# Optimization experiments

Hardware: AMD Instinct MI355X
Metric: run time of the kernel (lower is better)

## Reference

```python
import jax, jax.numpy as jnp
import numpy as np

MAX_VAL = 255.0
C1 = (0.01 * MAX_VAL) ** 2
C2 = (0.03 * MAX_VAL) ** 2


def _gauss_window(ws, sigma, channel=3):
    x = np.arange(ws, dtype=np.float64)
    g = np.exp(-((x - ws // 2) ** 2) / (2.0 * sigma ** 2))
    g = g / g.sum()
    w2 = np.outer(g, g).astype(np.float32)  # [ws, ws]
    w = np.broadcast_to(w2, (channel, 1, ws, ws)).copy()  # depthwise OIHW
    return jnp.asarray(w)


def _dwconv(x, w, pad):
    # depthwise conv2d, NCHW, groups == channels
    return jax.lax.conv_general_dilated(
        x, w, window_strides=(1, 1), padding=[(pad, pad), (pad, pad)],
        dimension_numbers=("NCHW", "OIHW", "NCHW"),
        feature_group_count=x.shape[1])


def _ssim_pair(img1, img2):
    _, c, h, w = img1.shape
    ws = min(h, w, 11)
    sigma = 1.5 * ws / 11.0
    win = _gauss_window(ws, sigma, c)
    pad = ws // 2
    mu1 = _dwconv(img1, win, pad)
    mu2 = _dwconv(img2, win, pad)
    mu1_sq, mu2_sq, mu1_mu2 = mu1 * mu1, mu2 * mu2, mu1 * mu2
    sigma1_sq = _dwconv(img1 * img1, win, pad) - mu1_sq
    sigma2_sq = _dwconv(img2 * img2, win, pad) - mu2_sq
    sigma12 = _dwconv(img1 * img2, win, pad) - mu1_mu2
    V1 = 2.0 * sigma12 + C2
    V2 = sigma1_sq + sigma2_sq + C2
    ssim_map = (2.0 * mu1_mu2 + C1) * V1 / ((mu1_sq + mu2_sq + C1) * V2)
    mcs_map = V1 / V2
    return ssim_map.mean(), mcs_map.mean()


def _avg_pool2(x):
    B, C, H, W = x.shape
    return x.reshape(B, C, H // 2, 2, W // 2, 2).mean(axis=(3, 5))


def _ms_ssim(img1, img2, levels=5):
    weight = jnp.array([0.0448, 0.2856, 0.3001, 0.2363, 0.1333], jnp.float32)
    msssim, mcs = [], []
    for _ in range(levels):
        s, m = _ssim_pair(img1, img2)
        msssim.append(s)
        mcs.append(m)
        img1 = _avg_pool2(img1)
        img2 = _avg_pool2(img2)
    msssim = jnp.stack(msssim)
    mcs = jnp.stack(mcs)
    value = jnp.prod(mcs[: levels - 1] ** weight[: levels - 1]) * msssim[levels - 1] ** weight[levels - 1]
    return 1.0 - value


def _l1_oss(img1, img2):
    _, c, h, w = img1.shape
    ws = min(h, w, 7)
    sigma = 1.1 * ws / 7.0
    win = _gauss_window(ws, sigma, c)
    return _dwconv(jnp.abs(img1 - img2), win, ws // 2).mean()


def _clr_loss(img1, img3):
    _, c, h, w = img1.shape
    ws = min(h, w, 29)
    sigma = ws / 6.0
    win = _gauss_window(ws, sigma, c)
    pad = ws // 2
    mu1 = _dwconv(img1, win, pad)
    mu3 = _dwconv(img3, win, pad)
    cw = [-0.000519, 0.07633, -0.173433, 1.435936, -1.894404, 1.556091]
    # Horner evaluation of cw[5]*x^5 + ... + cw[1]*x + cw[0]
    mu1 = ((((cw[5] * mu1 + cw[4]) * mu1 + cw[3]) * mu1 + cw[2]) * mu1 + cw[1]) * mu1 + cw[0]
    wgray = jnp.array([0.299, 0.587, 0.144], jnp.float32).reshape(1, 3, 1, 1)
    mug1 = (mu1 * wgray).sum(axis=1, keepdims=True)  # 1x1 conv over channels
    mug3 = (mu3 * wgray).sum(axis=1, keepdims=True)
    me1 = mug1.mean(axis=(2, 3), keepdims=True)
    me3 = mug3.mean(axis=(2, 3), keepdims=True)
    sc = me1 / me3
    return jnp.abs(mu1 - mu3 * sc).mean()


def setup_inputs() -> dict:
    key = jax.random.key(0)
    k1, k2, k3 = jax.random.split(key, 3)
    shape = (16, 3, 512, 512)
    return {
        "img1": jax.random.uniform(k1, shape, dtype=jnp.float32),
        "img2": jax.random.uniform(k2, shape, dtype=jnp.float32),
        "img3": jax.random.uniform(k3, shape, dtype=jnp.float32),
    }


def reference(img1, img2, img3):
    l1v = _l1_oss(img1, img2)
    clrv = _clr_loss(img1, img3)
    ssimv = _ms_ssim(img1, img2)
    return 0.4 * ssimv + 0.4 * l1v + 0.2 * clrv
```

## Files before the change

kernel.cpp:

```cpp
#include <hip/hip_runtime.h>
#include <hip/hip_fp16.h>
#include <cmath>

typedef float f2 __attribute__((ext_vector_type(2)));

struct GW7  { float g[7];  };
struct GW11 { float g[11]; };
struct GW29 { float g[29]; };

static void make_gauss(int ws, double sigma, float* out) {
    double t[32]; double s = 0.0;
    int c = ws / 2;
    for (int i = 0; i < ws; ++i) { double d = i - c; t[i] = exp(-(d * d) / (2.0 * sigma * sigma)); s += t[i]; }
    for (int i = 0; i < ws; ++i) out[i] = (float)(t[i] / s);
}

#define ACC_SLOTS 44
#define ACC_BYTES (ACC_SLOTS * 64 * sizeof(double))

__device__ __forceinline__ float poly5(float x) {
    float r = fmaf(1.556091f, x, -1.894404f);
    r = fmaf(r, x, 1.435936f);
    r = fmaf(r, x, -0.173433f);
    r = fmaf(r, x, 0.07633f);
    r = fmaf(r, x, -0.000519f);
    return r;
}

__device__ __forceinline__ float border7(int p, const GW7& gw) {
    if (p >= 3 && p <= 508) return 1.f;
    float r = 0.f;
    #pragma unroll
    for (int k = 0; k < 7; ++k) { int q = p + 3 - k; if (q >= 0 && q < 512) r += gw.g[k]; }
    return r;
}

#define SSP 49
#define SRP 33
template<bool INTER>
__global__ __launch_bounds__(256) void ssim_kernel(
    const float* __restrict__ Aim, const float* __restrict__ Bim, const f2* __restrict__ AB,
    int H, int tpp, int tilesX, GW11 gw, GW7 g7, double* __restrict__ acc, int level,
    f2* __restrict__ pooled, int Ho)
{
    constexpr int TILE = 32, IN = 42;
    __shared__ f2 lds[2 * IN * SRP];
    __shared__ float red[12];
    f2* s    = lds;
    f2* r_mu = lds;
    f2* r_sq = lds + IN * SRP;

    const int tid = threadIdx.x;
    const int bid = blockIdx.x;
    const int plane = bid / tpp;
    const int t = bid - plane * tpp;
    const int ty = t / tilesX, tx = t - ty * tilesX;
    const size_t base = (size_t)plane * H * H;
    const int oy = ty * TILE - 5, ox = tx * TILE - 5;

    for (int i = tid; i < IN * IN; i += 256) {
        int y = i / IN, x = i - y * IN;
        int gy = oy + y, gx = ox + x;
        bool ok = (gy >= 0) && (gy < H) && (gx >= 0) && (gx < H);
        size_t o = base + (size_t)gy * H + gx;
        f2 v = {0.f, 0.f};
        if (ok) {
            if (INTER) v = AB[o];
            else { v.x = Aim[o]; v.y = Bim[o]; }
        }
        s[y * SSP + x] = v;
    }
    __syncthreads();

    f2 v[18];
    const int ry = tid >> 2, rx0 = (tid & 3) * 8;
    if (tid < IN * 4) {
        #pragma unroll
        for (int l = 0; l < 18; ++l) v[l] = s[ry * SSP + rx0 + l];
    }
    if (pooled) {
        int py = tid >> 4, px = tid & 15;
        int a = (5 + 2 * py) * SSP + 5 + 2 * px;
        f2 u = s[a] + s[a + 1] + s[a + SSP] + s[a + SSP + 1];
        pooled[(size_t)plane * Ho * Ho + (size_t)(ty * 16 + py) * Ho + (tx * 16 + px)] = 0.25f * u;
    }
    float l1p = 0.f;
    if (level == 0) {
        #pragma unroll
        for (int jj = 0; jj < 4; ++jj) {
            int p = jj * 256 + tid;
            int py = p >> 5, px = p & 31;
            f2 u = s[(5 + py) * SSP + 5 + px];
            float w = border7(ty * 32 + py, g7) * border7(tx * 32 + px, g7);
            l1p += w * fabsf(u.x - u.y);
        }
    }
    __syncthreads();

    if (tid < IN * 4) {
        #pragma unroll
        for (int j = 0; j < 8; ++j) {
            f2 a = {0.f, 0.f};
            #pragma unroll
            for (int k = 0; k < 11; ++k) a = gw.g[k] * v[j + k] + a;
            r_mu[ry * SRP + rx0 + j] = a;
        }
        #pragma unroll
        for (int l = 0; l < 18; ++l) {
            f2 w;
            w.x = fmaf(v[l].x, v[l].x, v[l].y * v[l].y);
            w.y = v[l].x * v[l].y;
            v[l] = w;
        }
        #pragma unroll
        for (int j = 0; j < 8; ++j) {
            f2 a = {0.f, 0.f};
            #pragma unroll
            for (int k = 0; k < 11; ++k) a = gw.g[k] * v[j + k] + a;
            r_sq[ry * SRP + rx0 + j] = a;
        }
    }
    __syncthreads();

    const int y0 = (tid >> 5) * 4, x = tid & 31;
    float lss = 0.f, lmc = 0.f;
    {
        f2 mu[4], q[4];
        {
            f2 u[14];
            #pragma unroll
            for (int l = 0; l < 14; ++l) u[l] = r_mu[(y0 + l) * SRP + x];
            #pragma unroll
            for (int j = 0; j < 4; ++j) {
                f2 a = {0.f, 0.f};
                #pragma unroll
                for (int k = 0; k < 11; ++k) a = gw.g[k] * u[j + k] + a;
                mu[j] = a;
            }
        }
        {
            f2 u[14];
            #pragma unroll
            for (int l = 0; l < 14; ++l) u[l] = r_sq[(y0 + l) * SRP + x];
            #pragma unroll
            for (int j = 0; j < 4; ++j) {
                f2 a = {0.f, 0.f};
                #pragma unroll
                for (int k = 0; k < 11; ++k) a = gw.g[k] * u[j + k] + a;
                q[j] = a;
            }
        }
        #pragma unroll
        for (int j = 0; j < 4; ++j) {
            float m1 = mu[j].x, m2 = mu[j].y;
            float P = m1 * m2;
            float S = fmaf(m1, m1, m2 * m2);
            float V1 = 2.f * (q[j].y - P) + 58.5225f;
            float V2 = (q[j].x - S) + 58.5225f;
            float num = (2.f * P + 6.5025f) * V1;
            float SC = S + 6.5025f;
            float inv = __builtin_amdgcn_rcpf(SC * V2);
            lss = fmaf(num, inv, lss);
            lmc = fmaf(V1 * SC, inv, lmc);
        }
    }
    #pragma unroll
    for (int o = 32; o > 0; o >>= 1) {
        lss += __shfl_down(lss, o); lmc += __shfl_down(lmc, o); l1p += __shfl_down(l1p, o);
    }
    if ((tid & 63) == 0) {
        int g = tid >> 6;
        red[g * 3] = lss; red[g * 3 + 1] = lmc; red[g * 3 + 2] = l1p;
    }
    __syncthreads();
    if (tid == 0) {
        float a = red[0] + red[3] + red[6] + red[9];
        float m = red[1] + red[4] + red[7] + red[10];
        int stripe = bid & 63;
        atomicAdd(&acc[(0 + level) * 64 + stripe], (double)a);
        atomicAdd(&acc[(5 + level) * 64 + stripe], (double)m);
        if (level == 0) {
            float l1 = red[2] + red[5] + red[8] + red[11];
            atomicAdd(&acc[10 * 64 + stripe], (double)l1);
        }
    }
}

#define CRP 33
template<int MODE>
__global__ __launch_bounds__(256) void clr_conv(
    const float* __restrict__ img1, const float* __restrict__ img3,
    __half2* __restrict__ pbuf, GW29 gw, double* __restrict__ acc)
{
    __shared__ f2 r[60 * CRP];
    __shared__ float red[8];
    __shared__ float sc_sh;

    const int tid = threadIdx.x, bid = blockIdx.x;
    const int plane = bid >> 8, t = bid & 255;
    const int ty = t >> 4, tx = t & 15;
    const int b = plane / 3, c = plane - b * 3;
    const float wg = (c == 0) ? 0.299f : (c == 1 ? 0.587f : 0.144f);
    const size_t base = (size_t)plane * (512 * 512);

    if (MODE == 2 && tid < 64) {
        double m1 = acc[(12 + b) * 64 + tid];
        double m3 = acc[(28 + b) * 64 + tid];
        #pragma unroll
        for (int o = 32; o > 0; o >>= 1) { m1 += __shfl_down(m1, o); m3 += __shfl_down(m3, o); }
        if (tid == 0) sc_sh = (float)(m1 / m3);
    }

    if (tid < 240) {
        const int ry = tid >> 2, xq = tid & 3;
        const int gy = ty * 32 - 14 + ry;
        const bool vr = (gy >= 0) && (gy < 512);
        const int c0 = tx * 8 + xq * 2 - 4;
        const float4* row1 = (const float4*)(img1 + base + (size_t)(vr ? gy : 0) * 512);
        const float4* row3 = (const float4*)(img3 + base + (size_t)(vr ? gy : 0) * 512);
        float w[40];
        float o1[8];
        #pragma unroll
        for (int k = 0; k < 10; ++k) {
            int cc = c0 + k;
            float4 f = {0.f, 0.f, 0.f, 0.f};
            if (vr && cc >= 0 && cc < 128) f = row1[cc];
            w[4 * k] = f.x; w[4 * k + 1] = f.y; w[4 * k + 2] = f.z; w[4 * k + 3] = f.w;
        }
        #pragma unroll
        for (int j = 0; j < 8; ++j) {
            float a = 0.f;
            #pragma unroll
            for (int k = 0; k < 29; ++k) a = fmaf(gw.g[k], w[2 + j + k], a);
            o1[j] = a;
        }
        #pragma unroll
        for (int k = 0; k < 10; ++k) {
            int cc = c0 + k;
            float4 f = {0.f, 0.f, 0.f, 0.f};
            if (vr && cc >= 0 && cc < 128) f = row3[cc];
            w[4 * k] = f.x; w[4 * k + 1] = f.y; w[4 * k + 2] = f.z; w[4 * k + 3] = f.w;
        }
        #pragma unroll
        for (int j = 0; j < 8; ++j) {
            float a = 0.f;
            #pragma unroll
            for (int k = 0; k < 29; ++k) a = fmaf(gw.g[k], w[2 + j + k], a);
            r[ry * CRP + xq * 8 + j] = (f2){o1[j], a};
        }
    }
    __syncthreads();

    const int y0 = (tid >> 5) * 4, x = tid & 31;
    f2 mu[4];
    {
        f2 u[32];
        #pragma unroll
        for (int l = 0; l < 32; ++l) u[l] = r[(y0 + l) * CRP + x];
        #pragma unroll
        for (int j = 0; j < 4; ++j) {
            f2 a = {0.f, 0.f};
            #pragma unroll
            for (int k = 0; k < 29; ++k) a = gw.g[k] * u[j + k] + a;
            mu[j] = a;
        }
    }
    float p1 = 0.f, p3 = 0.f;
    #pragma unroll
    for (int j = 0; j < 4; ++j) {
        float p = poly5(mu[j].x);
        if (MODE == 2) {
            p1 += fabsf(p - mu[j].y * sc_sh);
        } else {
            p1 += p; p3 += mu[j].y;
            if (MODE == 0)
                pbuf[base + (size_t)(ty * 32 + y0 + j) * 512 + (tx * 32 + x)] =
                    __floats2half2_rn(p, mu[j].y);
        }
    }
    if (MODE != 2) { p1 *= wg; p3 *= wg; }
    #pragma unroll
    for (int o = 32; o > 0; o >>= 1) { p1 += __shfl_down(p1, o); p3 += __shfl_down(p3, o); }
    if ((tid & 63) == 0) { red[(tid >> 6) * 2] = p1; red[(tid >> 6) * 2 + 1] = p3; }
    __syncthreads();
    if (tid == 0) {
        float a1 = red[0] + red[2] + red[4] + red[6];
        int stripe = bid & 63;
        if (MODE == 2) {
            atomicAdd(&acc[11 * 64 + stripe], (double)a1);
        } else {
            float a3 = red[1] + red[3] + red[5] + red[7];
            atomicAdd(&acc[(12 + b) * 64 + stripe], (double)a1);
            atomicAdd(&acc[(28 + b) * 64 + stripe], (double)a3);
        }
    }
}

__global__ __launch_bounds__(256) void clr_fin(
    const __half2* __restrict__ pbuf, double* __restrict__ acc)
{
    __shared__ float red[4];
    __shared__ float sc_sh;
    const int tid = threadIdx.x, bid = blockIdx.x;
    const int b = bid / 192, sub = bid - b * 192;
    if (tid < 64) {
        double m1 = acc[(12 + b) * 64 + tid];
        double m3 = acc[(28 + b) * 64 + tid];
        #pragma unroll
        for (int o = 32; o > 0; o >>= 1) { m1 += __shfl_down(m1, o); m3 += __shfl_down(m3, o); }
        if (tid == 0) sc_sh = (float)(m1 / m3);
    }
    __syncthreads();
    const float sc = sc_sh;
    const size_t bo = (size_t)b * 786432 + (size_t)sub * 4096;
    float s = 0.f;
    #pragma unroll
    for (int it = 0; it < 8; ++it) {
        size_t i = bo + it * 512 + tid * 2;
        float2 a = __half22float2(pbuf[i]);
        float2 c = __half22float2(pbuf[i + 1]);
        s += fabsf(a.x - a.y * sc) + fabsf(c.x - c.y * sc);
    }
    #pragma unroll
    for (int o = 32; o > 0; o >>= 1) s += __shfl_down(s, o);
    if ((tid & 63) == 0) red[tid >> 6] = s;
    __syncthreads();
    if (tid == 0)
        atomicAdd(&acc[11 * 64 + (bid & 63)], (double)(red[0] + red[1] + red[2] + red[3]));
}

__global__ void finalize_kernel(const double* __restrict__ acc, float* __restrict__ out)
{
    __shared__ double sums[ACC_SLOTS];
    int t = threadIdx.x;
    if (t < ACC_SLOTS) {
        double s = 0.0;
        for (int i = 0; i < 64; ++i) s += acc[t * 64 + i];
        sums[t] = s;
    }
    __syncthreads();
    if (t == 0) {
        const double w[5] = {0.0448, 0.2856, 0.3001, 0.2363, 0.1333};
        double value = 1.0;
        for (int l = 0; l < 5; ++l) {
            double dim = (double)(512 >> l);
            double cnt = 48.0 * dim * dim;
            double mval = (l < 4) ? (sums[5 + l] / cnt) : (sums[l] / cnt);
            value *= pow(mval, w[l]);
        }
        double n0 = 48.0 * 512.0 * 512.0;
        double l1v = sums[10] / n0;
        double clrv = sums[11] / n0;
        out[0] = (float)(0.4 * (1.0 - value) + 0.4 * l1v + 0.2 * clrv);
    }
}

extern "C" void kernel_launch(void* const* d_in, const int* in_sizes, int n_in,
                              void* d_out, int out_size, void* d_ws, size_t ws_size,
                              hipStream_t stream)
{
    (void)in_sizes; (void)n_in; (void)out_size;
    const float* img1 = (const float*)d_in[0];
    const float* img2 = (const float*)d_in[1];
    const float* img3 = (const float*)d_in[2];
    float* out = (float*)d_out;
    double* acc = (double*)d_ws;

    GW11 g11; make_gauss(11, 1.5, g11.g);
    GW7  g7;  make_gauss(7, 1.1, g7.g);
    GW29 g29; make_gauss(29, 29.0 / 6.0, g29.g);

    hipMemsetAsync(d_ws, 0, ACC_BYTES, stream);

    f2* pyr = (f2*)((char*)d_ws + 32768);
    size_t offs[4];
    offs[0] = 0;
    offs[1] = offs[0] + (size_t)48 * 256 * 256;
    offs[2] = offs[1] + (size_t)48 * 128 * 128;
    offs[3] = offs[2] + (size_t)48 * 64 * 64;
    const size_t PYRF2 = offs[3] + (size_t)48 * 32 * 32;

    const f2* cur = nullptr;
    int H = 512;
    for (int l = 0; l < 5; ++l) {
        int tilesX = H / 32; int tpp = tilesX * tilesX;
        f2* pooled = (l < 4) ? (pyr + offs[l]) : nullptr;
        int Ho = H / 2;
        if (l == 0)
            ssim_kernel<false><<<48 * tpp, 256, 0, stream>>>(
                img1, img2, nullptr, H, tpp, tilesX, g11, g7, acc, l, pooled, Ho);
        else
            ssim_kernel<true><<<48 * tpp, 256, 0, stream>>>(
                nullptr, nullptr, cur, H, tpp, tilesX, g11, g7, acc, l, pooled, Ho);
        cur = pooled; H = Ho;
    }

    const size_t poff = 32768 + PYRF2 * sizeof(f2);
    const size_t PBYTES = (size_t)48 * 512 * 512 * sizeof(__half2);
    __half2* pbuf = (__half2*)((char*)d_ws + poff);
    if (ws_size >= poff + PBYTES) {
        clr_conv<0><<<12288, 256, 0, stream>>>(img1, img3, pbuf, g29, acc);
        clr_fin<<<3072, 256, 0, stream>>>(pbuf, acc);
    } else {
        clr_conv<1><<<12288, 256, 0, stream>>>(img1, img3, pbuf, g29, acc);
        clr_conv<2><<<12288, 256, 0, stream>>>(img1, img3, pbuf, g29, acc);
    }

    finalize_kernel<<<1, 64, 0, stream>>>(acc, out);
}
```

Baseline: 237.2 us.

## Stream clr conv over full column strips with a ring buffer to avoid halo recompute

Each block of the 29-tap color-loss convolution now processes a whole 32-wide column strip. It slides down 512 rows and keeps horizontally convolved rows in a 128-row shared-memory ring buffer, instead of recomputing a 28-row halo for every 32x32 tile. This removes most of the redundant horizontal convolution work and global reads. In exchange the grid shrinks from 12288 to 768 blocks, adds per-chunk barriers, and uses more shared memory, which reduces parallelism and latency hiding.

```diff
diff --git a/kernel.cpp b/kernel.cpp
--- a/kernel.cpp
+++ b/kernel.cpp
@@ -187,18 +187,18 @@
 }
 
 #define CRP 33
+#define RING 128
 template<int MODE>
 __global__ __launch_bounds__(256) void clr_conv(
     const float* __restrict__ img1, const float* __restrict__ img3,
     __half2* __restrict__ pbuf, GW29 gw, double* __restrict__ acc)
 {
-    __shared__ f2 r[60 * CRP];
+    __shared__ f2 r[RING * CRP];
     __shared__ float red[8];
     __shared__ float sc_sh;
 
     const int tid = threadIdx.x, bid = blockIdx.x;
-    const int plane = bid >> 8, t = bid & 255;
-    const int ty = t >> 4, tx = t & 15;
+    const int plane = bid >> 4, tx = bid & 15;
     const int b = plane / 3, c = plane - b * 3;
     const float wg = (c == 0) ? 0.299f : (c == 1 ? 0.587f : 0.144f);
     const size_t base = (size_t)plane * (512 * 512);
@@ -211,20 +211,25 @@
         if (tid == 0) sc_sh = (float)(m1 / m3);
     }
 
-    if (tid < 240) {
-        const int ry = tid >> 2, xq = tid & 3;
-        const int gy = ty * 32 - 14 + ry;
-        const bool vr = (gy >= 0) && (gy < 512);
-        const int c0 = tx * 8 + xq * 2 - 4;
-        const float4* row1 = (const float4*)(img1 + base + (size_t)(vr ? gy : 0) * 512);
-        const float4* row3 = (const float4*)(img3 + base + (size_t)(vr ? gy : 0) * 512);
+    const int rrow = tid >> 2, xq = tid & 3;
+    const int c0 = tx * 8 + xq * 2 - 4;
+
+    auto rowconv = [&](int lr) {
+        const int ri = ((lr + RING) & (RING - 1)) * CRP + xq * 8;
+        if (lr < 0 || lr >= 512) {
+            #pragma unroll
+            for (int j = 0; j < 8; ++j) r[ri + j] = (f2){0.f, 0.f};
+            return;
+        }
+        const float4* row1 = (const float4*)(img1 + base + (size_t)lr * 512);
+        const float4* row3 = (const float4*)(img3 + base + (size_t)lr * 512);
         float w[40];
         float o1[8];
         #pragma unroll
         for (int k = 0; k < 10; ++k) {
             int cc = c0 + k;
             float4 f = {0.f, 0.f, 0.f, 0.f};
-            if (vr && cc >= 0 && cc < 128) f = row1[cc];
+            if (cc >= 0 && cc < 128) f = row1[cc];
             w[4 * k] = f.x; w[4 * k + 1] = f.y; w[4 * k + 2] = f.z; w[4 * k + 3] = f.w;
         }
         #pragma unroll
@@ -238,7 +243,7 @@
         for (int k = 0; k < 10; ++k) {
             int cc = c0 + k;
             float4 f = {0.f, 0.f, 0.f, 0.f};
-            if (vr && cc >= 0 && cc < 128) f = row3[cc];
+            if (cc >= 0 && cc < 128) f = row3[cc];
             w[4 * k] = f.x; w[4 * k + 1] = f.y; w[4 * k + 2] = f.z; w[4 * k + 3] = f.w;
         }
         #pragma unroll
@@ -246,38 +251,48 @@
             float a = 0.f;
             #pragma unroll
             for (int k = 0; k < 29; ++k) a = fmaf(gw.g[k], w[2 + j + k], a);
-            r[ry * CRP + xq * 8 + j] = (f2){o1[j], a};
-        }
-    }
-    __syncthreads();
-
-    const int y0 = (tid >> 5) * 4, x = tid & 31;
-    f2 mu[4];
-    {
-        f2 u[32];
-        #pragma unroll
-        for (int l = 0; l < 32; ++l) u[l] = r[(y0 + l) * CRP + x];
-        #pragma unroll
-        for (int j = 0; j < 4; ++j) {
-            f2 a = {0.f, 0.f};
-            #pragma unroll
-            for (int k = 0; k < 29; ++k) a = gw.g[k] * u[j + k] + a;
-            mu[j] = a;
-        }
-    }
+            r[ri + j] = (f2){o1[j], a};
+        }
+    };
+
+    rowconv(-14 + rrow);
+    __syncthreads();
+
     float p1 = 0.f, p3 = 0.f;
-    #pragma unroll
-    for (int j = 0; j < 4; ++j) {
-        float p = poly5(mu[j].x);
-        if (MODE == 2) {
-            p1 += fabsf(p - mu[j].y * sc_sh);
-        } else {
-            p1 += p; p3 += mu[j].y;
-            if (MODE == 0)
-                pbuf[base + (size_t)(ty * 32 + y0 + j) * 512 + (tx * 32 + x)] =
-                    __floats2half2_rn(p, mu[j].y);
-        }
-    }
+    const int x = tid & 31;
+    #pragma unroll 1
+    for (int ck = 0; ck < 8; ++ck) {
+        {
+            int lr = 50 + 64 * ck + rrow;
+            if (lr <= 525) rowconv(lr);
+        }
+        __syncthreads();
+        #pragma unroll
+        for (int g = 0; g < 2; ++g) {
+            const int y0 = 64 * ck + g * 32 + (tid >> 5) * 4;
+            f2 u[32];
+            #pragma unroll
+            for (int l = 0; l < 32; ++l)
+                u[l] = r[(((y0 - 14 + l) + RING) & (RING - 1)) * CRP + x];
+            #pragma unroll
+            for (int j = 0; j < 4; ++j) {
+                f2 a = {0.f, 0.f};
+                #pragma unroll
+                for (int k = 0; k < 29; ++k) a = gw.g[k] * u[j + k] + a;
+                float p = poly5(a.x);
+                if (MODE == 2) {
+                    p1 += fabsf(p - a.y * sc_sh);
+                } else {
+                    p1 += p; p3 += a.y;
+                    if (MODE == 0)
+                        pbuf[base + (size_t)(y0 + j) * 512 + (tx * 32 + x)] =
+                            __floats2half2_rn(p, a.y);
+                }
+            }
+        }
+        if (ck < 7) __syncthreads();
+    }
+
     if (MODE != 2) { p1 *= wg; p3 *= wg; }
     #pragma unroll
     for (int o = 32; o > 0; o >>= 1) { p1 += __shfl_down(p1, o); p3 += __shfl_down(p3, o); }
@@ -399,11 +414,11 @@
     const size_t PBYTES = (size_t)48 * 512 * 512 * sizeof(__half2);
     __half2* pbuf = (__half2*)((char*)d_ws + poff);
     if (ws_size >= poff + PBYTES) {
-        clr_conv<0><<<12288, 256, 0, stream>>>(img1, img3, pbuf, g29, acc);
+        clr_conv<0><<<768, 256, 0, stream>>>(img1, img3, pbuf, g29, acc);
         clr_fin<<<3072, 256, 0, stream>>>(pbuf, acc);
     } else {
-        clr_conv<1><<<12288, 256, 0, stream>>>(img1, img3, pbuf, g29, acc);
-        clr_conv<2><<<12288, 256, 0, stream>>>(img1, img3, pbuf, g29, acc);
+        clr_conv<1><<<768, 256, 0, stream>>>(img1, img3, pbuf, g29, acc);
+        clr_conv<2><<<768, 256, 0, stream>>>(img1, img3, pbuf, g29, acc);
     }
 
     finalize_kernel<<<1, 64, 0, stream>>>(acc, out);
```

New measurement: 223.4 us. 1.06x faster.
